# Kernel optimization log

Measured on AMD Instinct MI355X. Metric: run time of the kernel, lower is better.

## Reference

```python
import jax, jax.numpy as jnp
import numpy as np

N, D = 8192, 1024


def setup_inputs() -> dict:
    key = jax.random.key(0)
    k1, k2 = jax.random.split(key)
    source = jax.random.normal(k1, (N, D), dtype=jnp.float32)
    target = jax.random.normal(k2, (N, D), dtype=jnp.float32)
    return {"source": source, "target": target}


def reference(source, target):
    # delta: [N, D]; loss = mean over all N*N entries of delta @ delta.T
    delta = source - target
    gram = jnp.matmul(delta, delta.T)  # [N, N]
    return jnp.mean(gram)
```

## Files before the change

kernel.cpp:

```cpp
#include <hip/hip_runtime.h>


#define MMD_N 8192
#define MMD_D 1024
#define NREP 16
#define CS_BLOCKS 256
#define CS_THREADS 1024
#define TEAMS 4
#define ROWS_PER_TEAM 8

__global__ __launch_bounds__(256) void mmd_zero_ws(float* __restrict__ ws) {
    float4* w4 = reinterpret_cast<float4*>(ws);
#pragma unroll
    for (int i = 0; i < NREP; ++i)
        w4[i * 256 + threadIdx.x] = make_float4(0.f, 0.f, 0.f, 0.f);
}

__global__ __launch_bounds__(CS_THREADS) void mmd_colsum(const float* __restrict__ src,
                                                         const float* __restrict__ tgt,
                                                         float* __restrict__ ws) {
    const int tid  = threadIdx.x;
    const int team = tid >> 8;
    const int col4 = tid & 255;
    const int row0 = blockIdx.x * (TEAMS * ROWS_PER_TEAM) + team * ROWS_PER_TEAM;
    const float4* s4 = reinterpret_cast<const float4*>(src);
    const float4* t4 = reinterpret_cast<const float4*>(tgt);

    float4 s[ROWS_PER_TEAM], t[ROWS_PER_TEAM];
#pragma unroll
    for (int r = 0; r < ROWS_PER_TEAM; ++r) {
        const int idx = (row0 + r) * (MMD_D / 4) + col4;
        s[r] = s4[idx];
        t[r] = t4[idx];
    }
    float4 acc = make_float4(0.f, 0.f, 0.f, 0.f);
#pragma unroll
    for (int r = 0; r < ROWS_PER_TEAM; ++r) {
        acc.x += s[r].x - t[r].x;
        acc.y += s[r].y - t[r].y;
        acc.z += s[r].z - t[r].z;
        acc.w += s[r].w - t[r].w;
    }

    __shared__ float4 red[TEAMS][256];
    red[team][col4] = acc;
    __syncthreads();
    if (tid < 256) {
        float4 a = red[0][tid];
        float4 b = red[1][tid];
        float4 c = red[2][tid];
        float4 d = red[3][tid];
        float4 tot;
        tot.x = (a.x + b.x) + (c.x + d.x);
        tot.y = (a.y + b.y) + (c.y + d.y);
        tot.z = (a.z + b.z) + (c.z + d.z);
        tot.w = (a.w + b.w) + (c.w + d.w);
        float* wrep = ws + (blockIdx.x & (NREP - 1)) * MMD_D;
        atomicAdd(&wrep[4 * tid + 0], tot.x);
        atomicAdd(&wrep[4 * tid + 1], tot.y);
        atomicAdd(&wrep[4 * tid + 2], tot.z);
        atomicAdd(&wrep[4 * tid + 3], tot.w);
    }
}

__global__ __launch_bounds__(256) void mmd_finish(const float* __restrict__ ws,
                                                  float* __restrict__ out) {
    const int tid = threadIdx.x;
    const float4* w4 = reinterpret_cast<const float4*>(ws);
    float4 tot = make_float4(0.f, 0.f, 0.f, 0.f);
#pragma unroll
    for (int i = 0; i < NREP; ++i) {
        float4 v = w4[i * 256 + tid];
        tot.x += v.x; tot.y += v.y; tot.z += v.z; tot.w += v.w;
    }
    float sq = tot.x * tot.x + tot.y * tot.y + tot.z * tot.z + tot.w * tot.w;
    for (int off = 32; off > 0; off >>= 1)
        sq += __shfl_down(sq, off, 64);
    __shared__ float part[4];
    if ((tid & 63) == 0) part[tid >> 6] = sq;
    __syncthreads();
    if (tid == 0) {
        float totsq = part[0] + part[1] + part[2] + part[3];
        out[0] = totsq / ((float)MMD_N * (float)MMD_N);
    }
}

extern "C" void kernel_launch(void* const* d_in, const int* in_sizes, int n_in,
                              void* d_out, int out_size, void* d_ws, size_t ws_size,
                              hipStream_t stream) {
    const float* src = (const float*)d_in[0];
    const float* tgt = (const float*)d_in[1];
    float* out = (float*)d_out;
    float* ws = (float*)d_ws;

    mmd_zero_ws<<<1, 256, 0, stream>>>(ws);
    mmd_colsum<<<CS_BLOCKS, CS_THREADS, 0, stream>>>(src, tgt, ws);
    mmd_finish<<<1, 256, 0, stream>>>(ws, out);
}
```

Before: 25.92 us.

## Replace atomic column-sum accumulation with per-block partial stores and single-block reduce

Each of 512 blocks now writes its 1024-column partial sum directly to workspace. A single 1024-thread block then reduces all partials and computes the squared norm. This drops the workspace-zeroing launch and the contended atomics, and doubles the block count for more memory parallelism. In exchange the workspace is larger and the final reduction must read 2 MB serially in one block. An atomic fallback is kept for when the workspace is too small.

```diff
diff --git a/kernel.cpp b/kernel.cpp
--- a/kernel.cpp
+++ b/kernel.cpp
@@ -3,26 +3,20 @@
 
 #define MMD_N 8192
 #define MMD_D 1024
-#define NREP 16
-#define CS_BLOCKS 256
+
+#define CS_BLOCKS 512
 #define CS_THREADS 1024
 #define TEAMS 4
-#define ROWS_PER_TEAM 8
+#define ROWS_PER_BLOCK (MMD_N / CS_BLOCKS)
+#define ROWS_PER_TEAM (ROWS_PER_BLOCK / TEAMS)
 
-__global__ __launch_bounds__(256) void mmd_zero_ws(float* __restrict__ ws) {
-    float4* w4 = reinterpret_cast<float4*>(ws);
-#pragma unroll
-    for (int i = 0; i < NREP; ++i)
-        w4[i * 256 + threadIdx.x] = make_float4(0.f, 0.f, 0.f, 0.f);
-}
-
-__global__ __launch_bounds__(CS_THREADS) void mmd_colsum(const float* __restrict__ src,
-                                                         const float* __restrict__ tgt,
-                                                         float* __restrict__ ws) {
+__global__ __launch_bounds__(CS_THREADS) void mmd_colsum_store(
+    const float* __restrict__ src, const float* __restrict__ tgt,
+    float* __restrict__ ws) {
     const int tid  = threadIdx.x;
     const int team = tid >> 8;
     const int col4 = tid & 255;
-    const int row0 = blockIdx.x * (TEAMS * ROWS_PER_TEAM) + team * ROWS_PER_TEAM;
+    const int row0 = blockIdx.x * ROWS_PER_BLOCK + team * ROWS_PER_TEAM;
     const float4* s4 = reinterpret_cast<const float4*>(src);
     const float4* t4 = reinterpret_cast<const float4*>(tgt);
 
@@ -55,6 +49,95 @@
         tot.y = (a.y + b.y) + (c.y + d.y);
         tot.z = (a.z + b.z) + (c.z + d.z);
         tot.w = (a.w + b.w) + (c.w + d.w);
+        reinterpret_cast<float4*>(ws)[blockIdx.x * 256 + tid] = tot;
+    }
+}
+
+__global__ __launch_bounds__(1024) void mmd_finish_store(
+    const float* __restrict__ ws, float* __restrict__ out) {
+    const int tid  = threadIdx.x;
+    const int team = tid >> 8;
+    const int c    = tid & 255;
+    const float4* w4 = reinterpret_cast<const float4*>(ws);
+    float4 acc = make_float4(0.f, 0.f, 0.f, 0.f);
+#pragma unroll 8
+    for (int r = team * (CS_BLOCKS / TEAMS); r < (team + 1) * (CS_BLOCKS / TEAMS); ++r) {
+        float4 v = w4[r * 256 + c];
+        acc.x += v.x; acc.y += v.y; acc.z += v.z; acc.w += v.w;
+    }
+    __shared__ float4 red[TEAMS][256];
+    red[team][c] = acc;
+    __syncthreads();
+
+    float sq = 0.f;
+    if (tid < 256) {
+        float4 a = red[0][tid];
+        float4 b = red[1][tid];
+        float4 cc = red[2][tid];
+        float4 d = red[3][tid];
+        float4 tot;
+        tot.x = (a.x + b.x) + (cc.x + d.x);
+        tot.y = (a.y + b.y) + (cc.y + d.y);
+        tot.z = (a.z + b.z) + (cc.z + d.z);
+        tot.w = (a.w + b.w) + (cc.w + d.w);
+        sq = tot.x * tot.x + tot.y * tot.y + tot.z * tot.z + tot.w * tot.w;
+    }
+    for (int off = 32; off > 0; off >>= 1)
+        sq += __shfl_down(sq, off, 64);
+    __shared__ float part[4];
+    if (tid < 256 && (tid & 63) == 0) part[tid >> 6] = sq;
+    __syncthreads();
+    if (tid == 0) {
+        float totsq = part[0] + part[1] + part[2] + part[3];
+        out[0] = totsq / ((float)MMD_N * (float)MMD_N);
+    }
+}
+
+#define NREP 16
+#define FB_BLOCKS 256
+#define FB_ROWS_PER_TEAM 8
+
+__global__ __launch_bounds__(256) void mmd_zero_ws(float* __restrict__ ws) {
+    float4* w4 = reinterpret_cast<float4*>(ws);
+#pragma unroll
+    for (int i = 0; i < NREP; ++i)
+        w4[i * 256 + threadIdx.x] = make_float4(0.f, 0.f, 0.f, 0.f);
+}
+
+__global__ __launch_bounds__(1024) void mmd_colsum_atomic(
+    const float* __restrict__ src, const float* __restrict__ tgt,
+    float* __restrict__ ws) {
+    const int tid  = threadIdx.x;
+    const int team = tid >> 8;
+    const int col4 = tid & 255;
+    const int row0 = blockIdx.x * (TEAMS * FB_ROWS_PER_TEAM) + team * FB_ROWS_PER_TEAM;
+    const float4* s4 = reinterpret_cast<const float4*>(src);
+    const float4* t4 = reinterpret_cast<const float4*>(tgt);
+
+    float4 acc = make_float4(0.f, 0.f, 0.f, 0.f);
+#pragma unroll
+    for (int r = 0; r < FB_ROWS_PER_TEAM; ++r) {
+        const int idx = (row0 + r) * (MMD_D / 4) + col4;
+        float4 s = s4[idx];
+        float4 t = t4[idx];
+        acc.x += s.x - t.x;
+        acc.y += s.y - t.y;
+        acc.z += s.z - t.z;
+        acc.w += s.w - t.w;
+    }
+    __shared__ float4 red[TEAMS][256];
+    red[team][col4] = acc;
+    __syncthreads();
+    if (tid < 256) {
+        float4 a = red[0][tid];
+        float4 b = red[1][tid];
+        float4 c = red[2][tid];
+        float4 d = red[3][tid];
+        float4 tot;
+        tot.x = (a.x + b.x) + (c.x + d.x);
+        tot.y = (a.y + b.y) + (c.y + d.y);
+        tot.z = (a.z + b.z) + (c.z + d.z);
+        tot.w = (a.w + b.w) + (c.w + d.w);
         float* wrep = ws + (blockIdx.x & (NREP - 1)) * MMD_D;
         atomicAdd(&wrep[4 * tid + 0], tot.x);
         atomicAdd(&wrep[4 * tid + 1], tot.y);
@@ -63,8 +146,8 @@
     }
 }
 
-__global__ __launch_bounds__(256) void mmd_finish(const float* __restrict__ ws,
-                                                  float* __restrict__ out) {
+__global__ __launch_bounds__(256) void mmd_finish_atomic(
+    const float* __restrict__ ws, float* __restrict__ out) {
     const int tid = threadIdx.x;
     const float4* w4 = reinterpret_cast<const float4*>(ws);
     float4 tot = make_float4(0.f, 0.f, 0.f, 0.f);
@@ -93,7 +176,12 @@
     float* out = (float*)d_out;
     float* ws = (float*)d_ws;
 
-    mmd_zero_ws<<<1, 256, 0, stream>>>(ws);
-    mmd_colsum<<<CS_BLOCKS, CS_THREADS, 0, stream>>>(src, tgt, ws);
-    mmd_finish<<<1, 256, 0, stream>>>(ws, out);
+    if (ws_size >= (size_t)CS_BLOCKS * MMD_D * sizeof(float)) {
+        mmd_colsum_store<<<CS_BLOCKS, CS_THREADS, 0, stream>>>(src, tgt, ws);
+        mmd_finish_store<<<1, 1024, 0, stream>>>(ws, out);
+    } else {
+        mmd_zero_ws<<<1, 256, 0, stream>>>(ws);
+        mmd_colsum_atomic<<<FB_BLOCKS, 1024, 0, stream>>>(src, tgt, ws);
+        mmd_finish_atomic<<<1, 256, 0, stream>>>(ws, out);
+    }
 }
```

Result: slower. 36.54 us (+41.0%).

## Replace atomic column-sum replicas with per-block partials and parallel finale

Applied to the files above, without the earlier changes.

The colsum kernel now writes each block's per-column partial sums to its own workspace slot instead of doing atomic adds into 16 replicas. This removes the zero-initialization kernel. A new 64-block finale reduces the 256 partials per column group with wave shuffles, squares the result and atomically adds the scaled value into the output. The output is zeroed with a memset. This trades float atomics for a larger workspace (1 MB) that has to be read back, and spreads the final reduction across many blocks.

```diff
diff --git a/kernel.cpp b/kernel.cpp
--- a/kernel.cpp
+++ b/kernel.cpp
@@ -3,22 +3,15 @@
 
 #define MMD_N 8192
 #define MMD_D 1024
-#define NREP 16
 #define CS_BLOCKS 256
 #define CS_THREADS 1024
 #define TEAMS 4
 #define ROWS_PER_TEAM 8
+#define INV_N2 1.4901161193847656e-8f
 
-__global__ __launch_bounds__(256) void mmd_zero_ws(float* __restrict__ ws) {
-    float4* w4 = reinterpret_cast<float4*>(ws);
-#pragma unroll
-    for (int i = 0; i < NREP; ++i)
-        w4[i * 256 + threadIdx.x] = make_float4(0.f, 0.f, 0.f, 0.f);
-}
-
-__global__ __launch_bounds__(CS_THREADS) void mmd_colsum(const float* __restrict__ src,
-                                                         const float* __restrict__ tgt,
-                                                         float* __restrict__ ws) {
+__global__ __launch_bounds__(CS_THREADS) void mmd_colsum(
+    const float* __restrict__ src, const float* __restrict__ tgt,
+    float* __restrict__ ws) {
     const int tid  = threadIdx.x;
     const int team = tid >> 8;
     const int col4 = tid & 255;
@@ -26,20 +19,16 @@
     const float4* s4 = reinterpret_cast<const float4*>(src);
     const float4* t4 = reinterpret_cast<const float4*>(tgt);
 
-    float4 s[ROWS_PER_TEAM], t[ROWS_PER_TEAM];
+    float4 acc = make_float4(0.f, 0.f, 0.f, 0.f);
 #pragma unroll
     for (int r = 0; r < ROWS_PER_TEAM; ++r) {
         const int idx = (row0 + r) * (MMD_D / 4) + col4;
-        s[r] = s4[idx];
-        t[r] = t4[idx];
-    }
-    float4 acc = make_float4(0.f, 0.f, 0.f, 0.f);
-#pragma unroll
-    for (int r = 0; r < ROWS_PER_TEAM; ++r) {
-        acc.x += s[r].x - t[r].x;
-        acc.y += s[r].y - t[r].y;
-        acc.z += s[r].z - t[r].z;
-        acc.w += s[r].w - t[r].w;
+        float4 s = s4[idx];
+        float4 t = t4[idx];
+        acc.x += s.x - t.x;
+        acc.y += s.y - t.y;
+        acc.z += s.z - t.z;
+        acc.w += s.w - t.w;
     }
 
     __shared__ float4 red[TEAMS][256];
@@ -55,33 +44,33 @@
         tot.y = (a.y + b.y) + (c.y + d.y);
         tot.z = (a.z + b.z) + (c.z + d.z);
         tot.w = (a.w + b.w) + (c.w + d.w);
-        float* wrep = ws + (blockIdx.x & (NREP - 1)) * MMD_D;
-        atomicAdd(&wrep[4 * tid + 0], tot.x);
-        atomicAdd(&wrep[4 * tid + 1], tot.y);
-        atomicAdd(&wrep[4 * tid + 2], tot.z);
-        atomicAdd(&wrep[4 * tid + 3], tot.w);
+        reinterpret_cast<float4*>(ws)[blockIdx.x * 256 + tid] = tot;
     }
 }
 
-__global__ __launch_bounds__(256) void mmd_finish(const float* __restrict__ ws,
-                                                  float* __restrict__ out) {
-    const int tid = threadIdx.x;
+__global__ __launch_bounds__(256) void mmd_finale(
+    const float* __restrict__ ws, float* __restrict__ out) {
+    const int tid  = threadIdx.x;
+    const int j    = tid >> 6;
+    const int lane = tid & 63;
+    const int c    = blockIdx.x * 4 + j;
     const float4* w4 = reinterpret_cast<const float4*>(ws);
-    float4 tot = make_float4(0.f, 0.f, 0.f, 0.f);
+
+    float4 acc = make_float4(0.f, 0.f, 0.f, 0.f);
 #pragma unroll
-    for (int i = 0; i < NREP; ++i) {
-        float4 v = w4[i * 256 + tid];
-        tot.x += v.x; tot.y += v.y; tot.z += v.z; tot.w += v.w;
+    for (int k = 0; k < CS_BLOCKS / 64; ++k) {
+        float4 v = w4[(lane + 64 * k) * 256 + c];
+        acc.x += v.x; acc.y += v.y; acc.z += v.z; acc.w += v.w;
     }
-    float sq = tot.x * tot.x + tot.y * tot.y + tot.z * tot.z + tot.w * tot.w;
-    for (int off = 32; off > 0; off >>= 1)
-        sq += __shfl_down(sq, off, 64);
-    __shared__ float part[4];
-    if ((tid & 63) == 0) part[tid >> 6] = sq;
-    __syncthreads();
-    if (tid == 0) {
-        float totsq = part[0] + part[1] + part[2] + part[3];
-        out[0] = totsq / ((float)MMD_N * (float)MMD_N);
+    for (int off = 32; off > 0; off >>= 1) {
+        acc.x += __shfl_down(acc.x, off, 64);
+        acc.y += __shfl_down(acc.y, off, 64);
+        acc.z += __shfl_down(acc.z, off, 64);
+        acc.w += __shfl_down(acc.w, off, 64);
+    }
+    if (lane == 0) {
+        float sq = acc.x * acc.x + acc.y * acc.y + acc.z * acc.z + acc.w * acc.w;
+        atomicAdd(out, sq * INV_N2);
     }
 }
 
@@ -93,7 +82,7 @@
     float* out = (float*)d_out;
     float* ws = (float*)d_ws;
 
-    mmd_zero_ws<<<1, 256, 0, stream>>>(ws);
+    hipMemsetAsync(out, 0, sizeof(float), stream);
     mmd_colsum<<<CS_BLOCKS, CS_THREADS, 0, stream>>>(src, tgt, ws);
-    mmd_finish<<<1, 256, 0, stream>>>(ws, out);
+    mmd_finale<<<64, 256, 0, stream>>>(ws, out);
 }
```

After: 25.55 us. No clear change (-1.4%).
